# Optimization experiments

Measured on AMD Instinct MI355X. Metric: run time of the kernel, lower is better.

## Reference

```python
import jax, jax.numpy as jnp
import numpy as np

HEADS = 16
HEAD_DIM = 64


def _attn(q, k, v):
    # q: [..., Q, h, d], k/v: [..., K, h, d]  (non-causal SDPA, scale 1/sqrt(d))
    scale = 1.0 / np.sqrt(HEAD_DIM).astype(np.float32)
    s = jnp.einsum('...qhd,...khd->...hqk', q, k) * scale
    p = jax.nn.softmax(s, axis=-1)
    return jnp.einsum('...hqk,...khd->...qhd', p, v)


def setup_inputs() -> dict:
    key = jax.random.key(0)
    k0, k1, k2 = jax.random.split(key, 3)
    B, T, H, W, D = 4, 32, 16, 16, 1024
    inner = HEADS * HEAD_DIM
    x = jax.random.normal(k0, (B, T, H, W, D), jnp.float32)
    Wqkv = jax.random.normal(k1, (D, 3 * inner), jnp.float32) / np.sqrt(D)
    Wout = jax.random.normal(k2, (inner, D), jnp.float32) / np.sqrt(inner)
    bout = jnp.zeros((D,), jnp.float32)
    return {"x": x, "Wqkv": Wqkv, "Wout": Wout, "bout": bout, "reference_length": 3}


def reference(x, Wqkv, Wout, bout, reference_length):
    B, T, H, W, D = x.shape
    length = reference_length + 1
    n = T // length            # n_frames (chunks)
    S = H * W                  # tokens per frame
    h, d = HEADS, HEAD_DIM

    qkv = jnp.einsum('bthwD,De->bthwe', x, Wqkv)
    q, k, v = jnp.split(qkv, 3, axis=-1)

    def rs(t):  # -> [B, n, length, S, h, d]
        return t.reshape(B, n, length, S, h, d)

    qr, kr, vr = rs(q), rs(k), rs(v)

    # non-last chunks: query = first frame of chunk, keys/values = remaining r frames
    q_pre = qr[:, :-1, 0]                                             # [B, n-1, S, h, d]
    k_pre = kr[:, :-1, 1:].reshape(B, n - 1, reference_length * S, h, d)
    v_pre = vr[:, :-1, 1:].reshape(B, n - 1, reference_length * S, h, d)
    o_pre = _attn(q_pre, k_pre, v_pre).reshape(B, n - 1, H, W, h * d)

    # last chunk: all `length` frames are queries, keys/values = frames 1..length-1
    q_last = qr[:, -1].reshape(B, length * S, h, d)
    k_last = kr[:, -1, 1:].reshape(B, reference_length * S, h, d)
    v_last = vr[:, -1, 1:].reshape(B, reference_length * S, h, d)
    o_last = _attn(q_last, k_last, v_last).reshape(B, length, H, W, h * d)

    o = jnp.concatenate([o_pre, o_last], axis=1)  # [B, n-1+length, H, W, inner]
    return jnp.einsum('bthwe,eD->bthwD', o, Wout) + bout
```

## Files before the change

kernel.cpp:

```cpp
#include <hip/hip_runtime.h>
#include <hip/hip_bf16.h>

typedef __bf16 bf16;
typedef __bf16 bf16x8 __attribute__((ext_vector_type(8)));
typedef float  f32x4  __attribute__((ext_vector_type(4)));
typedef float  f32x4v __attribute__((ext_vector_type(4)));
typedef unsigned int u32x4 __attribute__((ext_vector_type(4)));

#define DEV __device__ __forceinline__

DEV void gload_lds16(const bf16* g, bf16* l) {
    __builtin_amdgcn_global_load_lds(
        (__attribute__((address_space(1))) void*)g,
        (__attribute__((address_space(3))) void*)l, 16, 0, 0);
}

DEV bf16x8 as_bf(u32x4 v) { return __builtin_bit_cast(bf16x8, v); }

DEV f32x4 mfma16(bf16x8 a, bf16x8 b, f32x4 c) {
    return __builtin_amdgcn_mfma_f32_16x16x32_bf16(a, b, c, 0, 0, 0);
}

constexpr int D_   = 1024;
constexpr int S_   = 256;
constexpr int TOUT = 11;
constexpr int MQ   = 4 * TOUT * S_;
constexpr int MKV  = 4 * 8 * 3 * S_;
constexpr int KVL  = 768;

__global__ void gather_q(const float* __restrict__ x, bf16* __restrict__ Aq) {
    const int idx  = blockIdx.x * 256 + threadIdx.x;
    const int row  = idx >> 7, part = idx & 127;
    const int b    = row / (TOUT * S_);
    const int r2   = row - b * (TOUT * S_);
    const int tout = r2 >> 8;
    const int s    = r2 & 255;
    const int tx   = tout < 7 ? tout * 4 : 28 + (tout - 7);
    const float* src = x + ((size_t)((b * 32 + tx) * S_ + s)) * D_ + part * 8;
    f32x4v v0 = *(const f32x4v*)src;
    f32x4v v1 = *(const f32x4v*)(src + 4);
    bf16x8 o;
    o[0]=(bf16)v0[0]; o[1]=(bf16)v0[1]; o[2]=(bf16)v0[2]; o[3]=(bf16)v0[3];
    o[4]=(bf16)v1[0]; o[5]=(bf16)v1[1]; o[6]=(bf16)v1[2]; o[7]=(bf16)v1[3];
    *(bf16x8*)(Aq + (size_t)row * D_ + part * 8) = o;
}

__global__ void gather_kv(const float* __restrict__ x, bf16* __restrict__ Akv) {
    const int idx = blockIdx.x * 256 + threadIdx.x;
    const int row = idx >> 7, part = idx & 127;
    const int b   = row / 6144;
    const int r2  = row - b * 6144;
    const int c   = r2 / KVL;
    const int j   = r2 - c * KVL;
    const int f   = 1 + (j >> 8);
    const int s   = j & 255;
    const int tx  = c * 4 + f;
    const float* src = x + ((size_t)((b * 32 + tx) * S_ + s)) * D_ + part * 8;
    f32x4v v0 = *(const f32x4v*)src;
    f32x4v v1 = *(const f32x4v*)(src + 4);
    bf16x8 o;
    o[0]=(bf16)v0[0]; o[1]=(bf16)v0[1]; o[2]=(bf16)v0[2]; o[3]=(bf16)v0[3];
    o[4]=(bf16)v1[0]; o[5]=(bf16)v1[1]; o[6]=(bf16)v1[2]; o[7]=(bf16)v1[3];
    *(bf16x8*)(Akv + (size_t)row * D_ + part * 8) = o;
}

__global__ void wtrans(const float* __restrict__ W, bf16* __restrict__ Wt, int N) {
    __shared__ float T[64][65];
    const int bid = blockIdx.x;
    const int kt = bid & 15, nt = bid >> 4;
    const int k0 = kt * 64, n0 = nt * 64;
    for (int i = 0; i < 16; ++i) {
        const int e = i * 256 + (int)threadIdx.x;
        const int kk = e >> 6, nn = e & 63;
        T[nn][kk] = W[(size_t)(k0 + kk) * N + n0 + nn];
    }
    __syncthreads();
    for (int i = 0; i < 16; ++i) {
        const int e = i * 256 + (int)threadIdx.x;
        const int n = e >> 6, kk = e & 63;
        Wt[(size_t)(n0 + n) * 1024 + k0 + kk] = (bf16)T[n][kk];
    }
}

__global__ void vtrans(const bf16* __restrict__ KV, bf16* __restrict__ Vt) {
    __shared__ bf16 T[64][66];
    const int bid = blockIdx.x;
    const int jt = bid % 12;
    const int h  = (bid / 12) & 15;
    const int bg = bid / 192;
    const int j0 = jt * 64;
    const bf16* src = KV + (size_t)bg * KVL * 2048 + 1024 + h * 64;
    for (int i = 0; i < 16; ++i) {
        const int e = i * 256 + (int)threadIdx.x;
        const int j = e >> 6, dd = e & 63;
        T[dd][j] = src[(size_t)(j0 + j) * 2048 + dd];
    }
    __syncthreads();
    bf16* dst = Vt + ((size_t)(bg * 16 + h)) * 64 * KVL;
    for (int i = 0; i < 16; ++i) {
        const int e = i * 256 + (int)threadIdx.x;
        const int d = e >> 6, jj = e & 63;
        dst[(size_t)d * KVL + j0 + jj] = T[d][jj];
    }
}

#define PH_MID() do { \
    __builtin_amdgcn_s_barrier(); \
    asm volatile("s_waitcnt lgkmcnt(0)" ::: "memory"); \
    __builtin_amdgcn_sched_barrier(0); \
    __builtin_amdgcn_s_setprio(1); \
} while(0)

#define PH_END() do { \
    __builtin_amdgcn_s_setprio(0); \
    __builtin_amdgcn_sched_barrier(0); \
    __builtin_amdgcn_s_barrier(); \
} while(0)

#define VM6() asm volatile("s_waitcnt vmcnt(6)" ::: "memory")

#define STAGE_A(bufc, half, tile) do { \
    const bf16* s0_ = pA + (size_t)(half) * 64 * 1024 + (tile) * 64; \
    bf16* d0_ = ldsA + (bufc) * 16384 + (half) * 8192; \
    gload_lds16(s0_, d0_); \
    gload_lds16(s0_ + (size_t)128 * 1024, d0_ + 4096); \
} while(0)

#define STAGE_B(bufc, half, tile) do { \
    const bf16* s0_ = pB + (size_t)(half) * 32 * 1024 + (tile) * 64; \
    bf16* d0_ = ldsB + (bufc) * 16384 + (half) * 8192; \
    gload_lds16(s0_, d0_); \
    gload_lds16(s0_ + (size_t)128 * 1024, d0_ + 4096); \
} while(0)

#define LDA(bufc, mh) do { \
    const bf16* p_ = sm + (bufc) * 16384 + (mh) * 8192; \
    _Pragma("unroll") \
    for (int j_ = 0; j_ < 4; ++j_) { \
        a[j_][0] = *(const u32x4*)(p_ + j_ * 1024 + eA0); \
        a[j_][1] = *(const u32x4*)(p_ + j_ * 1024 + eA1); \
    } \
} while(0)

#define LDB(bufc, nh) do { \
    const bf16* p_ = sm + 32768 + (bufc) * 16384 + (nh) * 8192; \
    _Pragma("unroll") \
    for (int j_ = 0; j_ < 2; ++j_) { \
        b[(nh)*2 + j_][0] = *(const u32x4*)(p_ + j_ * 1024 + eB0); \
        b[(nh)*2 + j_][1] = *(const u32x4*)(p_ + j_ * 1024 + eB1); \
    } \
} while(0)

#define MM(mh, nh) do { \
    _Pragma("unroll") \
    for (int j_ = 0; j_ < 4; ++j_) { \
        _Pragma("unroll") \
        for (int i_ = 0; i_ < 2; ++i_) { \
            f32x4 c_ = acc[(mh)*4 + j_][(nh)*2 + i_]; \
            c_ = mfma16(as_bf(a[j_][0]), as_bf(b[(nh)*2 + i_][0]), c_); \
            c_ = mfma16(as_bf(a[j_][1]), as_bf(b[(nh)*2 + i_][1]), c_); \
            acc[(mh)*4 + j_][(nh)*2 + i_] = c_; \
        } \
    } \
} while(0)

template<int EPI>
__global__ __launch_bounds__(512) void gemm8(
    const bf16* __restrict__ A, const bf16* __restrict__ Bt,
    bf16* __restrict__ Cb, float* __restrict__ Cf,
    const float* __restrict__ bias, int N, int mt, int nwg)
{
    __shared__ bf16 sm[65536];
    const int tid = threadIdx.x, lane = tid & 63, wid = tid >> 6;

    int wg = blockIdx.x;
    {
        const int q = nwg >> 3, r = nwg & 7, xcd = wg & 7, off = wg >> 3;
        wg = (xcd < r ? xcd * (q + 1) : r * (q + 1) + (xcd - r) * q) + off;
    }
    const int bm = wg % mt, bn = wg / mt;
    const int wr = wid >> 2, wc = wid & 3;
    const int l15 = lane & 15, l4 = lane >> 4;

    const int Rrow = (wid << 3) + (lane >> 3);
    const int G    = (lane & 7) ^ (lane >> 3);
    const bf16* pA = A  + (size_t)(bm * 256 + Rrow) * 1024 + G * 8;
    const int wc1 = Rrow >> 5, cc1 = Rrow & 31;
    const bf16* pB = Bt + (size_t)(bn * 256 + wc1 * 64 + cc1) * 1024 + G * 8;
    bf16* ldsA = sm + (wid << 9);
    bf16* ldsB = sm + 32768 + (wid << 9);

    const int g0  = l4 ^ (l15 & 7);
    const int eA0 = wr * 4096 + l15 * 64 + g0 * 8;
    const int eA1 = eA0 ^ 32;
    const int eB0 = wc * 2048 + l15 * 64 + g0 * 8;
    const int eB1 = eB0 ^ 32;

    f32x4 acc[8][4];
    u32x4 a[4][2], b[4][2];
    const f32x4 zf = {0.f, 0.f, 0.f, 0.f};
    #pragma unroll
    for (int m = 0; m < 8; ++m)
        #pragma unroll
        for (int n = 0; n < 4; ++n) acc[m][n] = zf;

    STAGE_A(0, 0, 0); STAGE_B(0, 0, 0); STAGE_B(0, 1, 0); STAGE_A(0, 1, 0);
    STAGE_A(1, 0, 1); STAGE_B(1, 0, 1); STAGE_B(1, 1, 1);
    asm volatile("s_waitcnt vmcnt(6)" ::: "memory");
    __builtin_amdgcn_s_barrier();

    #pragma unroll 1
    for (int t = 0; t < 8; ++t) {
        const int T1 = 2 * t + 1;
        const int n0 = (2 * t + 2 < 15) ? 2 * t + 2 : 15;
        const int n1 = (2 * t + 3 < 15) ? 2 * t + 3 : 15;
        LDA(0, 0); LDB(0, 0); STAGE_A(1, 1, T1);
        PH_MID(); MM(0, 0); PH_END();
        LDB(0, 1); STAGE_A(0, 0, n0);
        PH_MID(); MM(0, 1); PH_END();
        LDA(0, 1); STAGE_B(0, 0, n0);
        PH_MID(); MM(1, 0); PH_END();
        STAGE_B(0, 1, n0);
        PH_MID(); MM(1, 1); VM6(); PH_END();
        LDA(1, 0); LDB(1, 0); STAGE_A(0, 1, n0);
        PH_MID(); MM(0, 0); PH_END();
        LDB(1, 1); STAGE_A(1, 0, n1);
        PH_MID(); MM(0, 1); PH_END();
        LDA(1, 1); STAGE_B(1, 0, n1);
        PH_MID(); MM(1, 0); PH_END();
        STAGE_B(1, 1, n1);
        PH_MID(); MM(1, 1); VM6(); PH_END();
    }
    asm volatile("s_waitcnt vmcnt(0)" ::: "memory");

    #pragma unroll
    for (int m = 0; m < 8; ++m) {
        const int row = bm * 256 + wr * 128 + m * 16 + l4 * 4;
        #pragma unroll
        for (int n = 0; n < 4; ++n) {
            const int col = bn * 256 + wc * 64 + n * 16 + l15;
            f32x4 v = acc[m][n];
            if (EPI == 0) {
                #pragma unroll
                for (int r = 0; r < 4; ++r)
                    Cb[(size_t)(row + r) * N + col] = (bf16)v[r];
            } else {
                const float bs = bias[col];
                #pragma unroll
                for (int r = 0; r < 4; ++r)
                    Cf[(size_t)(row + r) * N + col] = v[r] + bs;
            }
        }
    }
}

__global__ __launch_bounds__(256, 3) void attn_fwd(
    const bf16* __restrict__ Q, const bf16* __restrict__ KV,
    const bf16* __restrict__ Vt, bf16* __restrict__ O)
{
    __shared__ bf16 Kl[2][64][32];
    __shared__ bf16 Vl[2][64][32];
    __shared__ bf16 Pl[4][16][88];

    const int tid = threadIdx.x, lane = tid & 63, wid = tid >> 6;
    int bid = blockIdx.x;
    const int h = bid & 15; bid >>= 4;
    const int qt = bid % 44, b = bid / 44;
    const int chunk = qt < 28 ? (qt >> 2) : 7;
    const int qrow0 = b * (TOUT * S_) +
                      (qt < 28 ? chunk * S_ + (qt & 3) * 64 : 7 * S_ + (qt - 28) * 64);

    const bf16* kg = KV + ((size_t)(b * 8 + chunk) * KVL) * 2048 + h * 64;
    const bf16* vg = Vt + ((size_t)((b * 8 + chunk) * 16 + h)) * 64 * KVL;

    const int l15 = lane & 15, l4 = lane >> 4;

    const int qrow = qrow0 + wid * 16 + l15;
    const bf16* qp = Q + (size_t)qrow * D_ + h * 64 + l4 * 8;
    const u32x4 q0 = *(const u32x4*)qp;
    const u32x4 q1 = *(const u32x4*)(qp + 32);

    float m_r[4], l_r[4], al[4];
    f32x4 oacc[4];
    const f32x4 zf = {0.f, 0.f, 0.f, 0.f};
    #pragma unroll
    for (int r = 0; r < 4; ++r) { m_r[r] = -1e30f; l_r[r] = 0.f; }
    #pragma unroll
    for (int n = 0; n < 4; ++n) oacc[n] = zf;

    const int ii = wid * 64 + lane;
    const int srow = ii >> 2, sc = ii & 3;
    bf16* kld = &Kl[0][0][0] + wid * 512;
    bf16* vld = &Vl[0][0][0] + wid * 512;
    const float scale = 0.125f;

    for (int kt = 0; kt < 12; ++kt) {
        const int kv0 = kt * 64;
        __syncthreads();
        gload_lds16(kg + (size_t)(kv0 + srow) * 2048 + sc * 8,      kld);
        gload_lds16(kg + (size_t)(kv0 + srow) * 2048 + 32 + sc * 8, kld + 2048);
        gload_lds16(vg + (size_t)srow * KVL + kv0 + sc * 8,         vld);
        gload_lds16(vg + (size_t)srow * KVL + kv0 + 32 + sc * 8,    vld + 2048);
        __syncthreads();

        f32x4 s[4];
        #pragma unroll
        for (int n = 0; n < 4; ++n) {
            const bf16* kp = &Kl[0][n * 16 + l15][l4 * 8];
            const u32x4 b0 = *(const u32x4*)kp;
            const u32x4 b1 = *(const u32x4*)(kp + 2048);
            f32x4 t = mfma16(as_bf(q0), as_bf(b0), zf);
            s[n] = mfma16(as_bf(q1), as_bf(b1), t);
        }

        #pragma unroll
        for (int r = 0; r < 4; ++r) {
            float v = fmaxf(fmaxf(s[0][r], s[1][r]), fmaxf(s[2][r], s[3][r]));
            #pragma unroll
            for (int off = 1; off <= 8; off <<= 1)
                v = fmaxf(v, __shfl_xor(v, off));
            const float mn = fmaxf(m_r[r], v * scale);
            al[r] = __expf(m_r[r] - mn);
            m_r[r] = mn;
            const float p0 = __expf(s[0][r] * scale - mn);
            const float p1 = __expf(s[1][r] * scale - mn);
            const float p2 = __expf(s[2][r] * scale - mn);
            const float p3 = __expf(s[3][r] * scale - mn);
            float sum = p0 + p1 + p2 + p3;
            #pragma unroll
            for (int off = 1; off <= 8; off <<= 1)
                sum += __shfl_xor(sum, off);
            l_r[r] = l_r[r] * al[r] + sum;
            Pl[wid][l4 * 4 + r][l15]      = (bf16)p0;
            Pl[wid][l4 * 4 + r][16 + l15] = (bf16)p1;
            Pl[wid][l4 * 4 + r][32 + l15] = (bf16)p2;
            Pl[wid][l4 * 4 + r][48 + l15] = (bf16)p3;
        }
        #pragma unroll
        for (int n = 0; n < 4; ++n)
            #pragma unroll
            for (int r = 0; r < 4; ++r) oacc[n][r] *= al[r];

        asm volatile("s_waitcnt lgkmcnt(0)" ::: "memory");

        #pragma unroll
        for (int kk = 0; kk < 2; ++kk) {
            const u32x4 pa = *(const u32x4*)(&Pl[wid][l15][kk * 32 + l4 * 8]);
            #pragma unroll
            for (int n = 0; n < 4; ++n) {
                const u32x4 bv = *(const u32x4*)(&Vl[kk][n * 16 + l15][l4 * 8]);
                oacc[n] = mfma16(as_bf(pa), as_bf(bv), oacc[n]);
            }
        }
    }

    #pragma unroll
    for (int r = 0; r < 4; ++r) {
        const float inv = 1.f / l_r[r];
        const size_t row = (size_t)(qrow0 + wid * 16 + l4 * 4 + r) * D_;
        #pragma unroll
        for (int n = 0; n < 4; ++n)
            O[row + h * 64 + n * 16 + l15] = (bf16)(oacc[n][r] * inv);
    }
}

extern "C" void kernel_launch(void* const* d_in, const int* in_sizes, int n_in,
                              void* d_out, int out_size, void* d_ws, size_t ws_size,
                              hipStream_t stream) {
    (void)in_sizes; (void)n_in; (void)out_size; (void)ws_size;
    const float* x    = (const float*)d_in[0];
    const float* Wqkv = (const float*)d_in[1];
    const float* Wout = (const float*)d_in[2];
    const float* bout = (const float*)d_in[3];

    bf16* Aq     = (bf16*)d_ws;
    bf16* Akv    = Aq     + (size_t)MQ  * 1024;
    bf16* Wqkv_t = Akv    + (size_t)MKV * 1024;
    bf16* Wout_t = Wqkv_t + (size_t)3072 * 1024;
    bf16* Qb     = Wout_t + (size_t)1024 * 1024;
    bf16* KVb    = Qb     + (size_t)MQ  * 1024;
    bf16* Vtb    = Akv;
    bf16* Ob     = Aq;

    gather_q <<<MQ  * 128 / 256, 256, 0, stream>>>(x, Aq);
    gather_kv<<<MKV * 128 / 256, 256, 0, stream>>>(x, Akv);
    wtrans<<<16 * 48, 256, 0, stream>>>(Wqkv, Wqkv_t, 3072);
    wtrans<<<16 * 16, 256, 0, stream>>>(Wout, Wout_t, 1024);

    gemm8<0><<<176, 512, 0, stream>>>(Aq, Wqkv_t, Qb, nullptr, nullptr,
                                      1024, 44, 176);
    gemm8<0><<<768, 512, 0, stream>>>(Akv, Wqkv_t + (size_t)1024 * 1024, KVb,
                                      nullptr, nullptr, 2048, 96, 768);

    vtrans<<<32 * 16 * 12, 256, 0, stream>>>(KVb, Vtb);
    attn_fwd<<<4 * 44 * 16, 256, 0, stream>>>(Qb, KVb, Vtb, Ob);

    gemm8<1><<<176, 512, 0, stream>>>(Ob, Wout_t, nullptr, (float*)d_out, bout,
                                      1024, 44, 176);
}
```

Before: 352.4 us.

## Double-buffer K/V tiles and keep P in registers via transposed attention MFMAs

The attention kernel now double-buffers K/V tiles in LDS, prefetching the next tile while the current one is computed, with one barrier per iteration. S is computed transposed (K as the A operand), so each lane holds a single query's scores and softmax needs only two cross-lane shuffles. P stays in registers through bf16 packing and ds_bpermute instead of a round trip through an LDS scratch buffer. Other changes: the 1/sqrt(d) scale is folded into Q, LDS reads use an XOR swizzle, output is staged through LDS for 16-byte coalesced stores, and occupancy is raised to 4. Scaling Q in bf16 before the matmul adds a little rounding, and the bpermute lane mapping is easy to get wrong.

```diff
diff --git a/kernel.cpp b/kernel.cpp
--- a/kernel.cpp
+++ b/kernel.cpp
@@ -19,6 +19,12 @@
 
 DEV f32x4 mfma16(bf16x8 a, bf16x8 b, f32x4 c) {
     return __builtin_amdgcn_mfma_f32_16x16x32_bf16(a, b, c, 0, 0, 0);
+}
+
+DEV int cvtpk(float lo, float hi) {
+    int r;
+    asm("v_cvt_pk_bf16_f32 %0, %1, %2" : "=v"(r) : "v"(lo), "v"(hi));
+    return r;
 }
 
 constexpr int D_   = 1024;
@@ -254,13 +260,12 @@
     }
 }
 
-__global__ __launch_bounds__(256, 3) void attn_fwd(
+__global__ __launch_bounds__(256, 4) void attn_fwd(
     const bf16* __restrict__ Q, const bf16* __restrict__ KV,
     const bf16* __restrict__ Vt, bf16* __restrict__ O)
 {
-    __shared__ bf16 Kl[2][64][32];
-    __shared__ bf16 Vl[2][64][32];
-    __shared__ bf16 Pl[4][16][88];
+    __shared__ bf16 Kl[2][2][64][32];
+    __shared__ bf16 Vl[2][2][64][32];
 
     const int tid = threadIdx.x, lane = tid & 63, wid = tid >> 6;
     int bid = blockIdx.x;
@@ -275,93 +280,131 @@
 
     const int l15 = lane & 15, l4 = lane >> 4;
 
-    const int qrow = qrow0 + wid * 16 + l15;
-    const bf16* qp = Q + (size_t)qrow * D_ + h * 64 + l4 * 8;
-    const u32x4 q0 = *(const u32x4*)qp;
-    const u32x4 q1 = *(const u32x4*)(qp + 32);
-
-    float m_r[4], l_r[4], al[4];
+    const bf16* qp = Q + (size_t)(qrow0 + wid * 16 + l15) * D_ + h * 64 + l4 * 8;
+    u32x4 q0, q1;
+    {
+        bf16x8 t0 = *(const bf16x8*)qp;
+        bf16x8 t1 = *(const bf16x8*)(qp + 32);
+        #pragma unroll
+        for (int j = 0; j < 8; ++j) {
+            t0[j] = (bf16)((float)t0[j] * 0.125f);
+            t1[j] = (bf16)((float)t1[j] * 0.125f);
+        }
+        q0 = __builtin_bit_cast(u32x4, t0);
+        q1 = __builtin_bit_cast(u32x4, t1);
+    }
+
+    const int R   = wid * 16 + (lane >> 2);
+    const int gsw = ((lane & 3) ^ ((lane >> 3) & 3)) * 8;
+    const int rg  = (l4 ^ ((l15 >> 1) & 3)) * 8;
+
+    const int baseA = ((2 * (l4 & 1)) * 16 + l15) * 4;
+    const int baseB = baseA + 64;
+    const bool hi2 = (l4 & 2) != 0;
+
+    float m_s = -1e30f, l_s = 0.f;
     f32x4 oacc[4];
     const f32x4 zf = {0.f, 0.f, 0.f, 0.f};
     #pragma unroll
-    for (int r = 0; r < 4; ++r) { m_r[r] = -1e30f; l_r[r] = 0.f; }
-    #pragma unroll
-    for (int n = 0; n < 4; ++n) oacc[n] = zf;
-
-    const int ii = wid * 64 + lane;
-    const int srow = ii >> 2, sc = ii & 3;
-    bf16* kld = &Kl[0][0][0] + wid * 512;
-    bf16* vld = &Vl[0][0][0] + wid * 512;
-    const float scale = 0.125f;
-
+    for (int m2 = 0; m2 < 4; ++m2) oacc[m2] = zf;
+
+#define ASTAGE(c, t) do { \
+    const int kv0_ = (t) * 64; \
+    gload_lds16(kg + (size_t)(kv0_ + R) * 2048 + gsw,      &Kl[c][0][0][0] + wid * 512); \
+    gload_lds16(kg + (size_t)(kv0_ + R) * 2048 + 32 + gsw, &Kl[c][1][0][0] + wid * 512); \
+    gload_lds16(vg + (size_t)R * KVL + kv0_ + gsw,         &Vl[c][0][0][0] + wid * 512); \
+    gload_lds16(vg + (size_t)R * KVL + kv0_ + 32 + gsw,    &Vl[c][1][0][0] + wid * 512); \
+} while (0)
+
+    ASTAGE(0, 0);
+    __syncthreads();
+
+    #pragma unroll 1
     for (int kt = 0; kt < 12; ++kt) {
-        const int kv0 = kt * 64;
-        __syncthreads();
-        gload_lds16(kg + (size_t)(kv0 + srow) * 2048 + sc * 8,      kld);
-        gload_lds16(kg + (size_t)(kv0 + srow) * 2048 + 32 + sc * 8, kld + 2048);
-        gload_lds16(vg + (size_t)srow * KVL + kv0 + sc * 8,         vld);
-        gload_lds16(vg + (size_t)srow * KVL + kv0 + 32 + sc * 8,    vld + 2048);
-        __syncthreads();
+        const int cur = kt & 1;
+        if (kt < 11) ASTAGE(cur ^ 1, kt + 1);
 
         f32x4 s[4];
         #pragma unroll
         for (int n = 0; n < 4; ++n) {
-            const bf16* kp = &Kl[0][n * 16 + l15][l4 * 8];
-            const u32x4 b0 = *(const u32x4*)kp;
-            const u32x4 b1 = *(const u32x4*)(kp + 2048);
-            f32x4 t = mfma16(as_bf(q0), as_bf(b0), zf);
-            s[n] = mfma16(as_bf(q1), as_bf(b1), t);
+            const bf16* kp = &Kl[cur][0][n * 16 + l15][0] + rg;
+            const u32x4 k0 = *(const u32x4*)kp;
+            const u32x4 k1 = *(const u32x4*)(kp + 2048);
+            f32x4 t = mfma16(as_bf(k0), as_bf(q0), zf);
+            s[n] = mfma16(as_bf(k1), as_bf(q1), t);
         }
 
-        #pragma unroll
-        for (int r = 0; r < 4; ++r) {
-            float v = fmaxf(fmaxf(s[0][r], s[1][r]), fmaxf(s[2][r], s[3][r]));
-            #pragma unroll
-            for (int off = 1; off <= 8; off <<= 1)
-                v = fmaxf(v, __shfl_xor(v, off));
-            const float mn = fmaxf(m_r[r], v * scale);
-            al[r] = __expf(m_r[r] - mn);
-            m_r[r] = mn;
-            const float p0 = __expf(s[0][r] * scale - mn);
-            const float p1 = __expf(s[1][r] * scale - mn);
-            const float p2 = __expf(s[2][r] * scale - mn);
-            const float p3 = __expf(s[3][r] * scale - mn);
-            float sum = p0 + p1 + p2 + p3;
-            #pragma unroll
-            for (int off = 1; off <= 8; off <<= 1)
-                sum += __shfl_xor(sum, off);
-            l_r[r] = l_r[r] * al[r] + sum;
-            Pl[wid][l4 * 4 + r][l15]      = (bf16)p0;
-            Pl[wid][l4 * 4 + r][16 + l15] = (bf16)p1;
-            Pl[wid][l4 * 4 + r][32 + l15] = (bf16)p2;
-            Pl[wid][l4 * 4 + r][48 + l15] = (bf16)p3;
-        }
+        float pm = s[0][0];
         #pragma unroll
         for (int n = 0; n < 4; ++n)
             #pragma unroll
-            for (int r = 0; r < 4; ++r) oacc[n][r] *= al[r];
-
-        asm volatile("s_waitcnt lgkmcnt(0)" ::: "memory");
+            for (int r = 0; r < 4; ++r) pm = fmaxf(pm, s[n][r]);
+        pm = fmaxf(pm, __shfl_xor(pm, 16));
+        pm = fmaxf(pm, __shfl_xor(pm, 32));
+        const float mn = fmaxf(m_s, pm);
+        const float al = __expf(m_s - mn);
+        m_s = mn;
+        float p[4][4];
+        float sum = 0.f;
+        #pragma unroll
+        for (int n = 0; n < 4; ++n)
+            #pragma unroll
+            for (int r = 0; r < 4; ++r) {
+                const float e = __expf(s[n][r] - mn);
+                p[n][r] = e; sum += e;
+            }
+        sum += __shfl_xor(sum, 16);
+        sum += __shfl_xor(sum, 32);
+        l_s = l_s * al + sum;
+        #pragma unroll
+        for (int m2 = 0; m2 < 4; ++m2) oacc[m2] *= al;
+
+        int u[4][2];
+        #pragma unroll
+        for (int n = 0; n < 4; ++n) {
+            u[n][0] = cvtpk(p[n][0], p[n][1]);
+            u[n][1] = cvtpk(p[n][2], p[n][3]);
+        }
 
         #pragma unroll
         for (int kk = 0; kk < 2; ++kk) {
-            const u32x4 pa = *(const u32x4*)(&Pl[wid][l15][kk * 32 + l4 * 8]);
+            const int e0 = __builtin_amdgcn_ds_bpermute(baseA, u[2 * kk][0]);
+            const int f0 = __builtin_amdgcn_ds_bpermute(baseA, u[2 * kk + 1][0]);
+            const int e1 = __builtin_amdgcn_ds_bpermute(baseA, u[2 * kk][1]);
+            const int f1 = __builtin_amdgcn_ds_bpermute(baseA, u[2 * kk + 1][1]);
+            const int e2 = __builtin_amdgcn_ds_bpermute(baseB, u[2 * kk][0]);
+            const int f2 = __builtin_amdgcn_ds_bpermute(baseB, u[2 * kk + 1][0]);
+            const int e3 = __builtin_amdgcn_ds_bpermute(baseB, u[2 * kk][1]);
+            const int f3 = __builtin_amdgcn_ds_bpermute(baseB, u[2 * kk + 1][1]);
+            u32x4 pb;
+            pb[0] = (unsigned)(hi2 ? f0 : e0);
+            pb[1] = (unsigned)(hi2 ? f1 : e1);
+            pb[2] = (unsigned)(hi2 ? f2 : e2);
+            pb[3] = (unsigned)(hi2 ? f3 : e3);
             #pragma unroll
-            for (int n = 0; n < 4; ++n) {
-                const u32x4 bv = *(const u32x4*)(&Vl[kk][n * 16 + l15][l4 * 8]);
-                oacc[n] = mfma16(as_bf(pa), as_bf(bv), oacc[n]);
+            for (int m2 = 0; m2 < 4; ++m2) {
+                const u32x4 vf = *(const u32x4*)(&Vl[cur][kk][m2 * 16 + l15][0] + rg);
+                oacc[m2] = mfma16(as_bf(vf), as_bf(pb), oacc[m2]);
             }
         }
-    }
-
+        __syncthreads();
+    }
+#undef ASTAGE
+
+    const float inv = 1.f / l_s;
+    bf16* sc = &Kl[0][0][0][0] + wid * 1152;
     #pragma unroll
-    for (int r = 0; r < 4; ++r) {
-        const float inv = 1.f / l_r[r];
-        const size_t row = (size_t)(qrow0 + wid * 16 + l4 * 4 + r) * D_;
-        #pragma unroll
-        for (int n = 0; n < 4; ++n)
-            O[row + h * 64 + n * 16 + l15] = (bf16)(oacc[n][r] * inv);
-    }
+    for (int m2 = 0; m2 < 4; ++m2)
+        #pragma unroll
+        for (int r = 0; r < 4; ++r)
+            sc[l15 * 72 + m2 * 16 + l4 * 4 + r] = (bf16)(oacc[m2][r] * inv);
+    const int rq = lane >> 2, rd = (lane & 3) * 16;
+    const bf16* sr = sc + rq * 72 + rd;
+    const u32x4 o0 = *(const u32x4*)sr;
+    const u32x4 o1 = *(const u32x4*)(sr + 8);
+    bf16* op = O + (size_t)(qrow0 + wid * 16 + rq) * D_ + h * 64 + rd;
+    *(u32x4*)op = o0;
+    *(u32x4*)(op + 8) = o1;
 }
 
 extern "C" void kernel_launch(void* const* d_in, const int* in_sizes, int n_in,
```

After: 316.2 us. -10.3%, faster.
